# Performance work log

Measured on AMD Instinct MI355X. Metric: run time of the kernel, lower is better.

## Reference

```python
import jax, jax.numpy as jnp
import numpy as np

E, H, LQ, LC, B = 1024, 16, 1024, 512, 4
HD = E // H
FF = 4 * E
EPS = 1e-6


def _rope(x):
    # x: [B, H, L, D]; interleaved rotary embedding (lucidrains-style)
    D, L = x.shape[-1], x.shape[-2]
    inv_freq = 1.0 / (10000.0 ** (jnp.arange(0, D, 2, dtype=jnp.float32) / D))
    ang = jnp.arange(L, dtype=jnp.float32)[:, None] * inv_freq[None, :]  # [L, D/2]
    cos, sin = jnp.cos(ang), jnp.sin(ang)
    x1, x2 = x[..., 0::2], x[..., 1::2]
    r1 = x1 * cos - x2 * sin
    r2 = x1 * sin + x2 * cos
    return jnp.stack([r1, r2], axis=-1).reshape(x.shape)


def _ln(x, w, b):
    mu = jnp.mean(x, -1, keepdims=True)
    var = jnp.mean(jnp.square(x - mu), -1, keepdims=True)
    return (x - mu) * jax.lax.rsqrt(var + EPS) * w + b


def _rope_attn(x, ctx, qw, qb, kw, kb, vw, vb, pw, pb, mask):
    Bn, L, Em = x.shape
    Lc = ctx.shape[1]
    q = (x @ qw.T + qb).reshape(Bn, L, H, HD).transpose(0, 2, 1, 3)
    k = (ctx @ kw.T + kb).reshape(Bn, Lc, H, HD).transpose(0, 2, 1, 3)
    v = (ctx @ vw.T + vb).reshape(Bn, Lc, H, HD).transpose(0, 2, 1, 3)
    q, k = _rope(q), _rope(k)
    s = jnp.einsum('bhic,bhjc->bhij', q, k) / np.sqrt(HD).astype(np.float32)
    if mask is not None:
        s = jnp.where(mask[None, None], -jnp.inf, s)
    p = jax.nn.softmax(s, axis=-1)
    o = jnp.einsum('bhij,bhjc->bhic', p, v)
    o = o.transpose(0, 2, 1, 3).reshape(Bn, L, Em)
    return o @ pw.T + pb


def setup_inputs() -> dict:
    key = jax.random.key(0)
    ks = iter(jax.random.split(key, 40))
    s = 0.02
    d = {}
    d['x'] = jax.random.normal(next(ks), (B, LQ, E), jnp.float32)
    d['context'] = jax.random.normal(next(ks), (B, LC, E), jnp.float32)
    d['attn_mask'] = jnp.triu(jnp.ones((LQ, LQ), bool), k=1)  # True = masked (causal)
    for g in ('g_msa', 'g_ca', 'g_mlp'):
        d[g] = jax.random.normal(next(ks), (1, 1, E), jnp.float32) * s
    for n in ('n1', 'n2', 'n3'):
        d[n + '_w'] = jnp.ones((E,), jnp.float32)
        d[n + '_b'] = jnp.zeros((E,), jnp.float32)
    for p in ('sa', 'ca'):
        for m in ('q', 'k', 'v', 'p'):
            d[f'{p}_{m}w'] = jax.random.normal(next(ks), (E, E), jnp.float32) * s
            d[f'{p}_{m}b'] = jnp.zeros((E,), jnp.float32)
    d['fc1_w'] = jax.random.normal(next(ks), (FF, E), jnp.float32) * s
    d['fc1_b'] = jnp.zeros((FF,), jnp.float32)
    d['fc2_w'] = jax.random.normal(next(ks), (E, FF), jnp.float32) * s
    d['fc2_b'] = jnp.zeros((E,), jnp.float32)
    return d


def reference(x, context, attn_mask,
              g_msa, g_ca, g_mlp,
              n1_w, n1_b, n2_w, n2_b, n3_w, n3_b,
              sa_qw, sa_qb, sa_kw, sa_kb, sa_vw, sa_vb, sa_pw, sa_pb,
              ca_qw, ca_qb, ca_kw, ca_kb, ca_vw, ca_vb, ca_pw, ca_pb,
              fc1_w, fc1_b, fc2_w, fc2_b):
    # self-attention (causal RoPE) with zero-init learned gate
    x = x + g_msa * _rope_attn(_ln(x, n1_w, n1_b), _ln(x, n1_w, n1_b),
                               sa_qw, sa_qb, sa_kw, sa_kb, sa_vw, sa_vb,
                               sa_pw, sa_pb, attn_mask)
    # cross-attention (RoPE on both streams, no mask)
    h = _ln(x, n2_w, n2_b)
    x = x + g_ca * _rope_attn(h, context,
                              ca_qw, ca_qb, ca_kw, ca_kb, ca_vw, ca_vb,
                              ca_pw, ca_pb, None)
    # gated MLP with tanh-approx GELU
    h = _ln(x, n3_w, n3_b)
    h = jax.nn.gelu(h @ fc1_w.T + fc1_b, approximate=True) @ fc2_w.T + fc2_b
    x = x + g_mlp * h
    return x
```

## Files before the change

### kernel.cpp

```cpp
#include <hip/hip_runtime.h>
#include <math.h>

#if !__has_builtin(__builtin_amdgcn_cvt_pk_fp8_f32)
#include <hip/hip_fp8.h>
#endif

typedef __attribute__((ext_vector_type(8))) short short8;
typedef __attribute__((ext_vector_type(4))) float f32x4;
typedef __attribute__((ext_vector_type(16))) float f32x16;
typedef unsigned char u8;
typedef unsigned short u16;
typedef unsigned int u32;
typedef __attribute__((ext_vector_type(2))) u32 u32x2;
typedef __attribute__((ext_vector_type(4))) u32 u32x4;
typedef __attribute__((ext_vector_type(8))) int i32x8;
typedef unsigned long long u64;

static constexpr int E = 1024, H = 16, LQ = 1024, LC = 512, Bn = 4, FF = 4096;
static constexpr int NTOK = Bn * LQ;
static constexpr int NCTX = Bn * LC;

#define QSCALE 0.1803368801111244f
#define DEFER_THR 11.5f

static constexpr size_t OFF_TCOS   = 0;
static constexpr size_t OFF_TSIN   = OFF_TCOS + (size_t)LQ*32*4;
static constexpr size_t OFF_BSAQKV = OFF_TSIN + (size_t)LQ*32*4;
static constexpr size_t OFF_BCAKV  = OFF_BSAQKV + 16384;
static constexpr size_t OFF_WSAQKV = OFF_BCAKV + 16384;
static constexpr size_t OFF_WSAP   = OFF_WSAQKV + (size_t)3072*1024*2;
static constexpr size_t OFF_WCAQ   = OFF_WSAP   + (size_t)1024*1024*2;
static constexpr size_t OFF_WCAKV  = OFF_WCAQ   + (size_t)1024*1024*2;
static constexpr size_t OFF_WCAP   = OFF_WCAKV  + (size_t)2048*1024*2;
static constexpr size_t OFF_WFC1   = OFF_WCAP   + (size_t)1024*1024*2;
static constexpr size_t OFF_WFC2   = OFF_WFC1   + (size_t)4096*1024*2;
static constexpr size_t OFF_CTXB   = OFF_WFC2   + (size_t)1024*4096*2;
static constexpr size_t OFF_H      = OFF_CTXB   + (size_t)2048*1024*2;
static constexpr size_t OFF_QKV    = OFF_H      + (size_t)4096*1024*2;
static constexpr size_t OFF_CAQ    = OFF_QKV;
static constexpr size_t OFF_CAKV   = OFF_QKV + (size_t)4096*1024*2;
static constexpr size_t OFF_QR     = OFF_QKV + (size_t)4096*3072*2;
static constexpr size_t OFF_KR     = OFF_QR  + (size_t)4096*1024*2;
static constexpr size_t OFF_VT     = OFF_KR  + (size_t)4096*1024*2;
static constexpr size_t OFF_AO     = OFF_VT  + (size_t)4096*1024*2;
static constexpr size_t OFF_U      = OFF_QKV;
static constexpr size_t WS_NEED    = OFF_AO + (size_t)4096*1024*2;

static __device__ __forceinline__ float bf2f(u16 u) {
  union { u32 i; float f; } un; un.i = ((u32)u) << 16; return un.f;
}
static __device__ __forceinline__ u16 f2bf(float f) {
  union { float f; u32 u; } un; un.f = f;
  u32 u = un.u;
  return (u16)((u + 0x7FFFu + ((u >> 16) & 1u)) >> 16);
}
static __device__ __forceinline__ u64 pack4(u16 a, u16 b, u16 c, u16 d) {
  return (u64)a | ((u64)b << 16) | ((u64)c << 32) | ((u64)d << 48);
}
static __device__ __forceinline__ f32x4 mfma16(short8 a, short8 b, f32x4 c) {
  return __builtin_amdgcn_mfma_f32_16x16x32_bf16(a, b, c, 0, 0, 0);
}
static __device__ __forceinline__ f32x16 mfma32(short8 a, short8 b, f32x16 c) {
  return __builtin_amdgcn_mfma_f32_32x32x16_bf16(a, b, c, 0, 0, 0);
}
static __device__ __forceinline__ void gload_lds16(void* lds, const void* g) {
  __builtin_amdgcn_global_load_lds(
      (const __attribute__((address_space(1))) void*)g,
      (__attribute__((address_space(3))) void*)lds, 16, 0, 0);
}
static __device__ __forceinline__ float gelu_tanh(float x) {
  float z2 = 1.5957691216057308f * (x + 0.044715f * x * x * x);
  float e = __expf(z2);
  float r = __builtin_amdgcn_rcpf(e + 1.0f);
  return x - x * r;
}
static __device__ __forceinline__ u32 cvtpk_bf16(float lo, float hi) {
  u32 r;
  asm("v_cvt_pk_bf16_f32 %0, %1, %2" : "=v"(r) : "v"(lo), "v"(hi));
  return r;
}
static __device__ __forceinline__ u32 pack_fp8x4(float a, float b, float c, float d) {
#if __has_builtin(__builtin_amdgcn_cvt_pk_fp8_f32)
  u32 r = (u32)__builtin_amdgcn_cvt_pk_fp8_f32(a, b, 0, false);
  r = (u32)__builtin_amdgcn_cvt_pk_fp8_f32(c, d, (int)r, true);
  return r;
#else
  __hip_fp8_e4m3 qa(a), qb(b), qc(c), qd(d);
  return (u32)qa.__x | ((u32)qb.__x << 8) | ((u32)qc.__x << 16) | ((u32)qd.__x << 24);
#endif
}
static __device__ __forceinline__ u8 fp8b(float f) {
#if __has_builtin(__builtin_amdgcn_cvt_pk_fp8_f32)
  return (u8)((u32)__builtin_amdgcn_cvt_pk_fp8_f32(f, f, 0, false) & 0xFFu);
#else
  __hip_fp8_e4m3 t(f); return t.__x;
#endif
}

__global__ __launch_bounds__(256) void build_tab(float* __restrict__ ct, float* __restrict__ st) {
  int idx = blockIdx.x * 256 + threadIdx.x;
  int pos = idx >> 5, i = idx & 31;
  float inv = powf(10000.f, -(float)i * (1.f / 32.f));
  float a = (float)pos * inv;
  ct[idx] = cosf(a);
  st[idx] = sinf(a);
}

struct Cvt11 { const float* s[11]; };
__global__ __launch_bounds__(256) void cvt_all(Cvt11 a, u16* __restrict__ dst) {
  u32 gid = blockIdx.x * 256 + threadIdx.x;
  u32 s, off;
  if (gid < 2097152u)      { s = gid >> 18;                        off = gid & 262143u; }
  else if (gid < 4194304u) { return; }
  else                     { s = 10;                               off = gid - 4194304u; }
  float4 v = *(const float4*)(a.s[s] + (size_t)off * 4);
  *(u64*)(dst + (size_t)gid * 4) = pack4(f2bf(v.x), f2bf(v.y), f2bf(v.z), f2bf(v.w));
}

__global__ __launch_bounds__(256) void cvt_fp8(const float* __restrict__ s0, const float* __restrict__ s1,
                                               u8* __restrict__ d0, u8* __restrict__ d1) {
  u32 gid = blockIdx.x * 256 + threadIdx.x;
  const float* s; u8* d; u32 off;
  if (gid < 1048576u) { s = s0; d = d0; off = gid; }
  else                { s = s1; d = d1; off = gid - 1048576u; }
  float4 v = *(const float4*)(s + (size_t)off * 4);
  *(u32*)(d + (size_t)off * 4) =
      pack_fp8x4(v.x * 256.f, v.y * 256.f, v.z * 256.f, v.w * 256.f);
}

struct Cp5 { const float* s[5]; };
__global__ __launch_bounds__(256) void copy5(Cp5 a, float* __restrict__ dst) {
  int gid = blockIdx.x * 256 + threadIdx.x;
  int s = gid >> 10, off = gid & 1023;
  int doff = (s < 3) ? s * 1024 : 4096 + (s - 3) * 1024;
  dst[doff + off] = a.s[s][off];
}

__global__ __launch_bounds__(256) void init_bias_gate(float* __restrict__ out, const float* __restrict__ bias,
                                                      const float* __restrict__ gate) {
  int i = (blockIdx.x * 256 + threadIdx.x) * 4;
  int c = i & 1023;
  float4 o = *(float4*)(out + i);
  o.x += gate[c] * bias[c];
  o.y += gate[c + 1] * bias[c + 1];
  o.z += gate[c + 2] * bias[c + 2];
  o.w += gate[c + 3] * bias[c + 3];
  *(float4*)(out + i) = o;
}

__global__ __launch_bounds__(256) void ln_bf16(const float* __restrict__ x, const float* __restrict__ w,
                                               const float* __restrict__ b, u16* __restrict__ out) {
  __shared__ float red[4];
  int row = blockIdx.x, tid = threadIdx.x;
  const float* xr = x + (size_t)row * 1024;
  float4 v = ((const float4*)xr)[tid];
  float s = v.x + v.y + v.z + v.w;
#pragma unroll
  for (int off = 32; off; off >>= 1) s += __shfl_xor(s, off);
  if ((tid & 63) == 0) red[tid >> 6] = s;
  __syncthreads();
  float mean = (red[0] + red[1] + red[2] + red[3]) * (1.f / 1024.f);
  float dx = v.x - mean, dy = v.y - mean, dz = v.z - mean, dw = v.w - mean;
  float sq = dx * dx + dy * dy + dz * dz + dw * dw;
#pragma unroll
  for (int off = 32; off; off >>= 1) sq += __shfl_xor(sq, off);
  __syncthreads();
  if ((tid & 63) == 0) red[tid >> 6] = sq;
  __syncthreads();
  float var = (red[0] + red[1] + red[2] + red[3]) * (1.f / 1024.f);
  float rstd = rsqrtf(var + 1e-6f);
  float4 wv = ((const float4*)w)[tid];
  float4 bv = ((const float4*)b)[tid];
  u64 o = pack4(f2bf(dx * rstd * wv.x + bv.x), f2bf(dy * rstd * wv.y + bv.y),
                f2bf(dz * rstd * wv.z + bv.z), f2bf(dw * rstd * wv.w + bv.w));
  *(u64*)(out + (size_t)row * 1024 + tid * 4) = o;
}

__global__ __launch_bounds__(256) void ln_fp8(const float* __restrict__ x, const float* __restrict__ w,
                                              const float* __restrict__ b, u8* __restrict__ out) {
  __shared__ float red[4];
  int row = blockIdx.x, tid = threadIdx.x;
  const float* xr = x + (size_t)row * 1024;
  float4 v = ((const float4*)xr)[tid];
  float s = v.x + v.y + v.z + v.w;
#pragma unroll
  for (int off = 32; off; off >>= 1) s += __shfl_xor(s, off);
  if ((tid & 63) == 0) red[tid >> 6] = s;
  __syncthreads();
  float mean = (red[0] + red[1] + red[2] + red[3]) * (1.f / 1024.f);
  float dx = v.x - mean, dy = v.y - mean, dz = v.z - mean, dw = v.w - mean;
  float sq = dx * dx + dy * dy + dz * dz + dw * dw;
#pragma unroll
  for (int off = 32; off; off >>= 1) sq += __shfl_xor(sq, off);
  __syncthreads();
  if ((tid & 63) == 0) red[tid >> 6] = sq;
  __syncthreads();
  float var = (red[0] + red[1] + red[2] + red[3]) * (1.f / 1024.f);
  float rstd = rsqrtf(var + 1e-6f);
  float4 wv = ((const float4*)w)[tid];
  float4 bv = ((const float4*)b)[tid];
  u32 pk = pack_fp8x4((dx * rstd * wv.x + bv.x) * 16.f, (dy * rstd * wv.y + bv.y) * 16.f,
                      (dz * rstd * wv.z + bv.z) * 16.f, (dw * rstd * wv.w + bv.w) * 16.f);
  *(u32*)(out + (size_t)row * 1024 + tid * 4) = pk;
}

struct RopeJob { const u16* src; u16* dst; int ld, col0, Lper, T, mode; float scale; };
struct Rope3 { RopeJob j[3]; };
__global__ __launch_bounds__(128) void rope3(Rope3 a, const float* __restrict__ cosT,
                                             const float* __restrict__ sinT) {
  RopeJob jb = a.j[blockIdx.y];
  int t = blockIdx.x;
  if (t >= jb.T) return;
  int b = t / jb.Lper, l = t - b * jb.Lper;
  int tid = threadIdx.x;
  int e0 = tid * 8;
  int h = e0 >> 6, d0 = e0 & 63;
  short8 vv = *(const short8*)(jb.src + (size_t)t * jb.ld + jb.col0 + e0);
  if (jb.mode == 0) {
    short8 ov;
#pragma unroll
    for (int j = 0; j < 4; ++j) {
      float x1 = bf2f((u16)vv[2 * j]);
      float x2 = bf2f((u16)vv[2 * j + 1]);
      int i = (d0 >> 1) + j;
      float c = cosT[l * 32 + i], s = sinT[l * 32 + i];
      ov[2 * j]     = (short)f2bf((x1 * c - x2 * s) * jb.scale);
      ov[2 * j + 1] = (short)f2bf((x1 * s + x2 * c) * jb.scale);
    }
    *(short8*)(jb.dst + (((size_t)b * H + h) * jb.Lper + l) * 64 + d0) = ov;
  } else {
#pragma unroll
    for (int m = 0; m < 8; ++m)
      jb.dst[(((size_t)b * H + h) * 64 + d0 + m) * jb.Lper + l] = (u16)vv[m];
  }
}

enum { EPI_BF16 = 0, EPI_GELU = 1, EPI_RESID = 2, EPI_ATOMIC = 3 };

template <int EPI>
__global__ __launch_bounds__(512, 4) void gemm2(const u16* __restrict__ A, const u16* __restrict__ W,
                                                const float* __restrict__ bias, u16* outb, float* outf,
                                                const float* res, const float* __restrict__ gate,
                                                int M, int N, int K, int kchunks) {
  __shared__ u16 As[2][128 * 64];
  __shared__ u16 Bs[2][128 * 64];

  int nwg = gridDim.x * gridDim.y;
  int bid = blockIdx.y * gridDim.x + blockIdx.x;
  int cpx = nwg >> 3;
  int swz = (bid & 7) * cpx + (bid >> 3);
  int bx = swz % gridDim.x;
  int by = swz / gridDim.x;
  int row0 = by * 128, col0 = bx * 128;

  const int Kc = K / kchunks;
  const int kbase = blockIdx.z * Kc;

  int tid = threadIdx.x;
  int lane = tid & 63, wid = tid >> 6;
  int wr = wid >> 2, wc = wid & 3;
  int lr = lane & 15, lg = lane >> 4;

  size_t a_off0, a_off1, b_off0, b_off1;
  int l_off0 = tid * 8, l_off1 = (512 + tid) * 8;
  {
    int q = tid, r = q >> 3, p = q & 7, sp = p ^ (r & 7);
    a_off0 = (size_t)(row0 + r) * K + sp * 8;
    b_off0 = (size_t)(col0 + r) * K + sp * 8;
    q = 512 + tid; r = q >> 3; p = q & 7; sp = p ^ (r & 7);
    a_off1 = (size_t)(row0 + r) * K + sp * 8;
    b_off1 = (size_t)(col0 + r) * K + sp * 8;
  }

  f32x4 acc[4][2] = {};

  const int nkt = Kc >> 6;
  {
    gload_lds16(&As[0][l_off0], A + a_off0 + kbase);
    gload_lds16(&Bs[0][l_off0], W + b_off0 + kbase);
    gload_lds16(&As[0][l_off1], A + a_off1 + kbase);
    gload_lds16(&Bs[0][l_off1], W + b_off1 + kbase);
  }
  __syncthreads();

  for (int kt = 0; kt < nkt; ++kt) {
    int cur = kt & 1;
    if (kt + 1 < nkt) {
      int k0 = kbase + ((kt + 1) << 6);
      gload_lds16(&As[cur ^ 1][l_off0], A + a_off0 + k0);
      gload_lds16(&Bs[cur ^ 1][l_off0], W + b_off0 + k0);
      gload_lds16(&As[cur ^ 1][l_off1], A + a_off1 + k0);
      gload_lds16(&Bs[cur ^ 1][l_off1], W + b_off1 + k0);
    }
#pragma unroll
    for (int kk = 0; kk < 2; ++kk) {
      short8 af[4], bfr[2];
#pragma unroll
      for (int m = 0; m < 4; ++m) {
        int r = wr * 64 + m * 16 + lr;
        int sc = (kk * 4 + lg) ^ (r & 7);
        af[m] = *(const short8*)(&As[cur][r * 64 + sc * 8]);
      }
#pragma unroll
      for (int n = 0; n < 2; ++n) {
        int r = wc * 32 + n * 16 + lr;
        int sc = (kk * 4 + lg) ^ (r & 7);
        bfr[n] = *(const short8*)(&Bs[cur][r * 64 + sc * 8]);
      }
#pragma unroll
      for (int m = 0; m < 4; ++m)
#pragma unroll
        for (int n = 0; n < 2; ++n)
          acc[m][n] = mfma16(af[m], bfr[n], acc[m][n]);
    }
    __syncthreads();
  }

  if (EPI == EPI_BF16 || EPI == EPI_GELU) {
    u16* Ct = &As[0][0];
#pragma unroll
    for (int n = 0; n < 2; ++n) {
      int c = wc * 32 + n * 16 + lr;
      float bv = bias[col0 + c];
#pragma unroll
      for (int m = 0; m < 4; ++m) {
#pragma unroll
        for (int i = 0; i < 4; ++i) {
          int r = wr * 64 + m * 16 + lg * 4 + i;
          float v = acc[m][n][i] + bv;
          Ct[r * 128 + c] = f2bf(EPI == EPI_GELU ? gelu_tanh(v) : v);
        }
      }
    }
    __syncthreads();
#pragma unroll
    for (int j = 0; j < 4; ++j) {
      u32 q = (u32)tid + j * 512;
      u32 r = q >> 4, ck = q & 15;
      short8 v = *(const short8*)(Ct + r * 128 + ck * 8);
      *(short8*)(outb + (size_t)(row0 + r) * N + col0 + ck * 8) = v;
    }
  } else {
#pragma unroll
    for (int n = 0; n < 2; ++n) {
      int cg = col0 + wc * 32 + n * 16 + lr;
      float bv = (EPI == EPI_ATOMIC) ? 0.f : bias[cg];
#pragma unroll
      for (int m = 0; m < 4; ++m) {
#pragma unroll
        for (int i = 0; i < 4; ++i) {
          int rg = row0 + wr * 64 + m * 16 + lg * 4 + i;
          float v = acc[m][n][i] + bv;
          if (EPI == EPI_RESID) {
            float r = res[(size_t)rg * N + cg];
            outf[(size_t)rg * N + cg] = r + gate[cg] * v;
          } else {
            atomicAdd(&outf[(size_t)rg * N + cg], gate[cg] * v);
          }
        }
      }
    }
  }
}

enum { E8_GELU = 0, E8_ATOMIC = 1 };

template <int EPI>
__global__ __launch_bounds__(256, 2) void gemm8(const u8* __restrict__ A, const u8* __restrict__ W,
                                                const float* __restrict__ bias, u8* outb, float* outf,
                                                const float* __restrict__ gate,
                                                int M, int N, int K, int kchunks) {
  __shared__ u8 As[2][128 * 128];
  __shared__ u8 Bs[2][128 * 128];

  int nwg = gridDim.x * gridDim.y;
  int bid = blockIdx.y * gridDim.x + blockIdx.x;
  int cpx = nwg >> 3;
  int swz = (bid & 7) * cpx + (bid >> 3);
  int bx = swz % gridDim.x, by = swz / gridDim.x;
  int row0 = by * 128, col0 = bx * 128;

  const int Kc = K / kchunks;
  const int kbase = blockIdx.z * Kc;

  int tid = threadIdx.x;
  int lane = tid & 63, wid = tid >> 6;
  int wr = wid >> 1, wc = wid & 1;
  int l31 = lane & 31, hi = lane >> 5;

  u32 aoff[4], boff[4];
  int ldso[4];
#pragma unroll
  for (int j = 0; j < 4; ++j) {
    int q = tid + j * 256;
    int r = q >> 3, p = q & 7, sp = p ^ (r & 7);
    aoff[j] = (u32)(row0 + r) * (u32)K + sp * 16;
    boff[j] = (u32)(col0 + r) * (u32)K + sp * 16;
    ldso[j] = q * 16;
  }

  f32x16 acc[2][2] = {};
  const int nkt = Kc >> 7;

  auto rdfrag = [&](const u8* base, int wbase, int ks, i32x8* f) {
#pragma unroll
    for (int blk = 0; blk < 2; ++blk) {
      int r = wbase + blk * 32 + l31;
      const u8* rp = base + r * 128;
      int ck = ks * 4 + hi * 2;
      u32x4 lo = *(const u32x4*)(rp + ((ck) ^ (r & 7)) * 16);
      u32x4 hh = *(const u32x4*)(rp + ((ck + 1) ^ (r & 7)) * 16);
      i32x8 v;
      v[0] = (int)lo[0]; v[1] = (int)lo[1]; v[2] = (int)lo[2]; v[3] = (int)lo[3];
      v[4] = (int)hh[0]; v[5] = (int)hh[1]; v[6] = (int)hh[2]; v[7] = (int)hh[3];
      f[blk] = v;
    }
  };

#pragma unroll
  for (int j = 0; j < 4; ++j) {
    gload_lds16(&As[0][ldso[j]], A + aoff[j] + kbase);
    gload_lds16(&Bs[0][ldso[j]], W + boff[j] + kbase);
  }
  __syncthreads();

  for (int kt = 0; kt < nkt; ++kt) {
    int cur = kt & 1;
    if (kt + 1 < nkt) {
      int k0 = kbase + ((kt + 1) << 7);
#pragma unroll
      for (int j = 0; j < 4; ++j) {
        gload_lds16(&As[cur ^ 1][ldso[j]], A + aoff[j] + k0);
        gload_lds16(&Bs[cur ^ 1][ldso[j]], W + boff[j] + k0);
      }
    }
#pragma unroll
    for (int ks = 0; ks < 2; ++ks) {
      i32x8 a[2], b[2];
      rdfrag(&As[cur][0], wr * 64, ks, a);
      rdfrag(&Bs[cur][0], wc * 64, ks, b);
      __builtin_amdgcn_s_setprio(1);
#pragma unroll
      for (int mi = 0; mi < 2; ++mi)
#pragma unroll
        for (int ni = 0; ni < 2; ++ni)
          acc[mi][ni] = __builtin_amdgcn_mfma_scale_f32_32x32x64_f8f6f4(
              a[mi], b[ni], acc[mi][ni], 0, 0, 0, 0x7F7F7F7F, 0, 0x7F7F7F7F);
      __builtin_amdgcn_s_setprio(0);
    }
    __syncthreads();
  }

  constexpr float SCL = 1.f / 4096.f;
  if (EPI == E8_GELU) {
    u8* Ct = &As[0][0];
#pragma unroll
    for (int ni = 0; ni < 2; ++ni) {
      int cl = wc * 64 + ni * 32 + l31;
      float bv = bias[col0 + cl];
#pragma unroll
      for (int mi = 0; mi < 2; ++mi) {
#pragma unroll
        for (int g = 0; g < 16; ++g) {
          int rl = wr * 64 + mi * 32 + (g & 3) + 8 * (g >> 2) + 4 * hi;
          float v = acc[mi][ni][g] * SCL + bv;
          Ct[rl * 128 + cl] = fp8b(gelu_tanh(v) * 16.f);
        }
      }
    }
    __syncthreads();
#pragma unroll
    for (int j = 0; j < 4; ++j) {
      int q = tid + j * 256;
      int r = q >> 3, ck = q & 7;
      *(u32x4*)(outb + (size_t)(row0 + r) * N + col0 + ck * 16) =
          *(const u32x4*)(Ct + r * 128 + ck * 16);
    }
  } else {
#pragma unroll
    for (int ni = 0; ni < 2; ++ni) {
      int cg = col0 + wc * 64 + ni * 32 + l31;
      float gv = gate[cg];
#pragma unroll
      for (int mi = 0; mi < 2; ++mi) {
#pragma unroll
        for (int g = 0; g < 16; ++g) {
          int rg = row0 + wr * 64 + mi * 32 + (g & 3) + 8 * (g >> 2) + 4 * hi;
          atomicAdd(&outf[(size_t)rg * N + cg], gv * (acc[mi][ni][g] * SCL));
        }
      }
    }
  }
}

template <int MASKED, int PRE>
static __device__ __forceinline__ void attn_tile3(short8* kf, const u16* KtNext,
                                                  const u16* Vp0, const u16* Vp1,
                                                  const short8* qf, int kb, int q0, int l31, int hi,
                                                  float& m, float& lsum, f32x16& o0, f32x16& o1) {
  short8 vf0[4], vf1[4];
#pragma unroll
  for (int ks = 0; ks < 4; ++ks) {
    vf0[ks] = *(const short8*)(Vp0 + ks * 16 + hi * 8);
    vf1[ks] = *(const short8*)(Vp1 + ks * 16 + hi * 8);
  }
  f32x16 s0 = {}, s1 = {};
  __builtin_amdgcn_s_setprio(1);
#pragma unroll
  for (int s = 0; s < 4; ++s) {
    s0 = mfma32(kf[s], qf[s], s0);
    s1 = mfma32(kf[4 + s], qf[s], s1);
  }
  __builtin_amdgcn_s_setprio(0);
  if (PRE) {
    const u16* kp0 = KtNext + (size_t)l31 * 64 + hi * 8;
    const u16* kp1 = KtNext + (size_t)(32 + l31) * 64 + hi * 8;
#pragma unroll
    for (int s = 0; s < 4; ++s) {
      kf[s] = *(const short8*)(kp0 + s * 16);
      kf[4 + s] = *(const short8*)(kp1 + s * 16);
    }
  }
  if (MASKED) {
    int qg = q0 + l31;
#pragma unroll
    for (int r = 0; r < 16; ++r) {
      int kk = kb + (r & 3) + 8 * (r >> 2) + 4 * hi;
      if (kk > qg) s0[r] = -INFINITY;
      if (kk + 32 > qg) s1[r] = -INFINITY;
    }
  }
  float pm = -INFINITY;
#pragma unroll
  for (int r = 0; r < 16; ++r) pm = fmaxf(pm, fmaxf(s0[r], s1[r]));
  pm = fmaxf(pm, __shfl_xor(pm, 32));
  if (!__all(pm <= m + DEFER_THR)) {
    float mn = fmaxf(m, pm);
    float al = exp2f(m - mn);
    m = mn;
    lsum *= al;
#pragma unroll
    for (int r = 0; r < 16; ++r) {
      float alr = __shfl(al, (r & 3) + 8 * (r >> 2) + 4 * hi);
      o0[r] *= alr;
      o1[r] *= alr;
    }
  }
  float ts = 0.f;
#pragma unroll
  for (int r = 0; r < 16; ++r) {
    float p0 = exp2f(s0[r] - m);
    float p1 = exp2f(s1[r] - m);
    s0[r] = p0; s1[r] = p1;
    ts += p0 + p1;
  }
  ts += __shfl_xor(ts, 32);
  lsum += ts;
  auto pack8 = [&](float a0, float a1, float a2, float a3,
                   float a4, float a5, float a6, float a7) -> short8 {
    u32 c0 = cvtpk_bf16(a0, a1), c1 = cvtpk_bf16(a2, a3);
    u32 c2 = cvtpk_bf16(a4, a5), c3 = cvtpk_bf16(a6, a7);
    u32x2 r02 = __builtin_amdgcn_permlane32_swap(c0, c2, false, false);
    u32x2 r13 = __builtin_amdgcn_permlane32_swap(c1, c3, false, false);
    u32x4 w;
    w[0] = r02[0]; w[1] = r13[0]; w[2] = r02[1]; w[3] = r13[1];
    return __builtin_bit_cast(short8, w);
  };
  short8 pa0 = pack8(s0[0], s0[1], s0[2], s0[3], s0[4], s0[5], s0[6], s0[7]);
  short8 pa1 = pack8(s0[8], s0[9], s0[10], s0[11], s0[12], s0[13], s0[14], s0[15]);
  short8 pa2 = pack8(s1[0], s1[1], s1[2], s1[3], s1[4], s1[5], s1[6], s1[7]);
  short8 pa3 = pack8(s1[8], s1[9], s1[10], s1[11], s1[12], s1[13], s1[14], s1[15]);
  short8 pa[4] = {pa0, pa1, pa2, pa3};
  __builtin_amdgcn_s_setprio(1);
#pragma unroll
  for (int ks = 0; ks < 4; ++ks) {
    o0 = mfma32(pa[ks], vf0[ks], o0);
    o1 = mfma32(pa[ks], vf1[ks], o1);
  }
  __builtin_amdgcn_s_setprio(0);
}

template <int CAUSAL>
__global__ __launch_bounds__(256) void flash_attn2(const u16* __restrict__ Q, const u16* __restrict__ K,
                                                   const u16* __restrict__ Vt, u16* __restrict__ O,
                                                   int Lq, int Lk) {
  const int wid = threadIdx.x >> 6, lane = threadIdx.x & 63;
  const int l31 = lane & 31, hi = lane >> 5;
  int wg = blockIdx.x * 4 + wid;
  int bh = wg & 63;
  int qc = wg >> 6;
  if (CAUSAL) qc = (Lq >> 5) - 1 - qc;
  int q0 = qc << 5;

  const u16* Qb = Q + ((size_t)bh * Lq + q0) * 64;
  const u16* Kb = K + (size_t)bh * Lk * 64;
  const u16* Vb = Vt + (size_t)bh * 64 * Lk;

  short8 qf[4];
#pragma unroll
  for (int s = 0; s < 4; ++s) qf[s] = *(const short8*)(Qb + (size_t)l31 * 64 + s * 16 + hi * 8);

  f32x16 o0 = {}, o1 = {};
  float m = -INFINITY, lsum = 0.f;

  const u16* Kt = Kb;
  const u16* Vp0 = Vb + (size_t)l31 * Lk;
  const u16* Vp1 = Vb + (size_t)(32 + l31) * Lk;

  short8 kf[8];
  {
    const u16* kp0 = Kt + (size_t)l31 * 64 + hi * 8;
    const u16* kp1 = Kt + (size_t)(32 + l31) * 64 + hi * 8;
#pragma unroll
    for (int s = 0; s < 4; ++s) {
      kf[s] = *(const short8*)(kp0 + s * 16);
      kf[4 + s] = *(const short8*)(kp1 + s * 16);
    }
  }

  int nt = CAUSAL ? ((q0 >> 6) + 1) : (Lk >> 6);
  for (int t = 0; t < nt - 1; ++t) {
    attn_tile3<0, 1>(kf, Kt + 64 * 64, Vp0, Vp1, qf, t * 64, q0, l31, hi, m, lsum, o0, o1);
    Kt += 64 * 64; Vp0 += 64; Vp1 += 64;
  }
  if (CAUSAL)
    attn_tile3<1, 0>(kf, nullptr, Vp0, Vp1, qf, (nt - 1) * 64, q0, l31, hi, m, lsum, o0, o1);
  else
    attn_tile3<0, 0>(kf, nullptr, Vp0, Vp1, qf, (nt - 1) * 64, q0, l31, hi, m, lsum, o0, o1);

  float myinv = 1.f / lsum;
  int b = bh >> 4, h = bh & 15;
#pragma unroll
  for (int r = 0; r < 16; ++r) {
    int cr = (r & 3) + 8 * (r >> 2) + 4 * hi;
    float li = __shfl(myinv, cr);
    u16* op = O + ((size_t)b * Lq + q0 + cr) * 1024 + h * 64;
    op[l31] = f2bf(o0[r] * li);
    op[32 + l31] = f2bf(o1[r] * li);
  }
}

extern "C" void kernel_launch(void* const* d_in, const int* in_sizes, int n_in,
                              void* d_out, int out_size, void* d_ws, size_t ws_size,
                              hipStream_t stream) {
  (void)in_sizes; (void)n_in; (void)out_size;
  if (ws_size < WS_NEED) return;

  const float* x     = (const float*)d_in[0];
  const float* ctx   = (const float*)d_in[1];
  const float* g_msa = (const float*)d_in[3];
  const float* g_ca  = (const float*)d_in[4];
  const float* g_mlp = (const float*)d_in[5];
  const float* n1w = (const float*)d_in[6],  *n1b = (const float*)d_in[7];
  const float* n2w = (const float*)d_in[8],  *n2b = (const float*)d_in[9];
  const float* n3w = (const float*)d_in[10], *n3b = (const float*)d_in[11];
  const float* sa_qw = (const float*)d_in[12], *sa_kw = (const float*)d_in[14];
  const float* sa_vw = (const float*)d_in[16], *sa_pw = (const float*)d_in[18];
  const float* sa_qb = (const float*)d_in[13], *sa_kb = (const float*)d_in[15];
  const float* sa_vb = (const float*)d_in[17], *sa_pb = (const float*)d_in[19];
  const float* ca_qw = (const float*)d_in[20], *ca_qb = (const float*)d_in[21];
  const float* ca_kw = (const float*)d_in[22], *ca_kb = (const float*)d_in[23];
  const float* ca_vw = (const float*)d_in[24], *ca_vb = (const float*)d_in[25];
  const float* ca_pw = (const float*)d_in[26], *ca_pb = (const float*)d_in[27];
  const float* fc1w = (const float*)d_in[28], *fc1b = (const float*)d_in[29];
  const float* fc2w = (const float*)d_in[30], *fc2b = (const float*)d_in[31];

  char* ws = (char*)d_ws;
  float* out = (float*)d_out;
  float* tcos = (float*)(ws + OFF_TCOS);
  float* tsin = (float*)(ws + OFF_TSIN);
  u16* Hb   = (u16*)(ws + OFF_H);
  u16* QKV  = (u16*)(ws + OFF_QKV);
  u16* QR   = (u16*)(ws + OFF_QR);
  u16* KR   = (u16*)(ws + OFF_KR);
  u16* VT   = (u16*)(ws + OFF_VT);
  u16* AO   = (u16*)(ws + OFF_AO);
  u8*  H8   = (u8*)(ws + OFF_H);
  u8*  U8   = (u8*)(ws + OFF_U);
  u8*  W8FC1 = (u8*)(ws + OFF_QR);
  u8*  W8FC2 = (u8*)(ws + OFF_KR);

  build_tab<<<dim3(128), dim3(256), 0, stream>>>(tcos, tsin);

  Cvt11 ca;
  ca.s[0] = sa_qw; ca.s[1] = sa_kw; ca.s[2] = sa_vw; ca.s[3] = sa_pw;
  ca.s[4] = ca_qw; ca.s[5] = ca_kw; ca.s[6] = ca_vw; ca.s[7] = ca_pw;
  ca.s[8] = fc1w;  ca.s[9] = fc2w;  ca.s[10] = ctx;
  cvt_all<<<dim3(18432), dim3(256), 0, stream>>>(ca, (u16*)(ws + OFF_WSAQKV));
  Cp5 cp;
  cp.s[0] = sa_qb; cp.s[1] = sa_kb; cp.s[2] = sa_vb; cp.s[3] = ca_kb; cp.s[4] = ca_vb;
  copy5<<<dim3(20), dim3(256), 0, stream>>>(cp, (float*)(ws + OFF_BSAQKV));

  ln_bf16<<<dim3(NTOK), dim3(256), 0, stream>>>(x, n1w, n1b, Hb);
  gemm2<EPI_BF16><<<dim3(3072 / 128, NTOK / 128), dim3(512), 0, stream>>>(
      Hb, (u16*)(ws + OFF_WSAQKV), (float*)(ws + OFF_BSAQKV), QKV, nullptr, nullptr, nullptr,
      NTOK, 3072, 1024, 1);
  {
    Rope3 r;
    r.j[0] = {QKV, QR, 3072, 0,    LQ, NTOK, 0, QSCALE};
    r.j[1] = {QKV, KR, 3072, 1024, LQ, NTOK, 0, 1.0f};
    r.j[2] = {QKV, VT, 3072, 2048, LQ, NTOK, 1, 1.0f};
    rope3<<<dim3(NTOK, 3), dim3(128), 0, stream>>>(r, tcos, tsin);
  }
  flash_attn2<1><<<dim3(512), dim3(256), 0, stream>>>(QR, KR, VT, AO, LQ, LQ);
  gemm2<EPI_RESID><<<dim3(1024 / 128, NTOK / 128), dim3(512), 0, stream>>>(
      AO, (u16*)(ws + OFF_WSAP), sa_pb, nullptr, out, x, g_msa, NTOK, 1024, 1024, 1);

  ln_bf16<<<dim3(NTOK), dim3(256), 0, stream>>>(out, n2w, n2b, Hb);
  gemm2<EPI_BF16><<<dim3(1024 / 128, NTOK / 128), dim3(512), 0, stream>>>(
      Hb, (u16*)(ws + OFF_WCAQ), ca_qb, (u16*)(ws + OFF_CAQ), nullptr, nullptr, nullptr,
      NTOK, 1024, 1024, 1);
  gemm2<EPI_BF16><<<dim3(2048 / 128, NCTX / 128), dim3(512), 0, stream>>>(
      (u16*)(ws + OFF_CTXB), (u16*)(ws + OFF_WCAKV), (float*)(ws + OFF_BCAKV),
      (u16*)(ws + OFF_CAKV), nullptr, nullptr, nullptr, NCTX, 2048, 1024, 1);
  {
    Rope3 r;
    r.j[0] = {(u16*)(ws + OFF_CAQ),  QR, 1024, 0,    LQ, NTOK, 0, QSCALE};
    r.j[1] = {(u16*)(ws + OFF_CAKV), KR, 2048, 0,    LC, NCTX, 0, 1.0f};
    r.j[2] = {(u16*)(ws + OFF_CAKV), VT, 2048, 1024, LC, NCTX, 1, 1.0f};
    rope3<<<dim3(NTOK, 3), dim3(128), 0, stream>>>(r, tcos, tsin);
  }
  flash_attn2<0><<<dim3(512), dim3(256), 0, stream>>>(QR, KR, VT, AO, LQ, LC);
  gemm2<EPI_RESID><<<dim3(1024 / 128, NTOK / 128), dim3(512), 0, stream>>>(
      AO, (u16*)(ws + OFF_WCAP), ca_pb, nullptr, out, out, g_ca, NTOK, 1024, 1024, 1);

  cvt_fp8<<<dim3(8192), dim3(256), 0, stream>>>(fc1w, fc2w, W8FC1, W8FC2);
  ln_fp8<<<dim3(NTOK), dim3(256), 0, stream>>>(out, n3w, n3b, H8);
  gemm8<E8_GELU><<<dim3(4096 / 128, NTOK / 128), dim3(256), 0, stream>>>(
      H8, W8FC1, fc1b, U8, nullptr, nullptr, NTOK, 4096, 1024, 1);
  init_bias_gate<<<dim3(4096), dim3(256), 0, stream>>>(out, fc2b, g_mlp);
  gemm8<E8_ATOMIC><<<dim3(1024 / 128, NTOK / 128, 2), dim3(256), 0, stream>>>(
      U8, W8FC2, nullptr, nullptr, out, g_mlp, NTOK, 1024, 4096, 2);
}
```

Baseline: 389.5 us.

## Replace split-K atomic FC2 with fused residual epilogue and 16x16x128 FP8 MFMA

The FC2 GEMM no longer uses a two-way split-K with atomicAdd plus a separate bias/gate init kernel. It now runs a single pass that writes residual + gate*(acc+bias) directly. The FP8 GEMM's inner loop also switches from 32x32x64 scaled MFMA to 16x16x128, with a 4x4 accumulator grid per wave, changing how fragments are read from LDS. Dropping split-K removes atomics and one kernel launch, but halves the FC2 grid to 256 blocks, which may underfill the GPU over the long K=4096 loop.

```diff
diff --git a/kernel.cpp b/kernel.cpp
--- a/kernel.cpp
+++ b/kernel.cpp
@@ -136,18 +136,6 @@
   dst[doff + off] = a.s[s][off];
 }
 
-__global__ __launch_bounds__(256) void init_bias_gate(float* __restrict__ out, const float* __restrict__ bias,
-                                                      const float* __restrict__ gate) {
-  int i = (blockIdx.x * 256 + threadIdx.x) * 4;
-  int c = i & 1023;
-  float4 o = *(float4*)(out + i);
-  o.x += gate[c] * bias[c];
-  o.y += gate[c + 1] * bias[c + 1];
-  o.z += gate[c + 2] * bias[c + 2];
-  o.w += gate[c + 3] * bias[c + 3];
-  *(float4*)(out + i) = o;
-}
-
 __global__ __launch_bounds__(256) void ln_bf16(const float* __restrict__ x, const float* __restrict__ w,
                                                const float* __restrict__ b, u16* __restrict__ out) {
   __shared__ float red[4];
@@ -235,13 +223,13 @@
   }
 }
 
-enum { EPI_BF16 = 0, EPI_GELU = 1, EPI_RESID = 2, EPI_ATOMIC = 3 };
+enum { EPI_BF16 = 0, EPI_GELU = 1, EPI_RESID = 2 };
 
 template <int EPI>
 __global__ __launch_bounds__(512, 4) void gemm2(const u16* __restrict__ A, const u16* __restrict__ W,
                                                 const float* __restrict__ bias, u16* outb, float* outf,
                                                 const float* res, const float* __restrict__ gate,
-                                                int M, int N, int K, int kchunks) {
+                                                int M, int N, int K) {
   __shared__ u16 As[2][128 * 64];
   __shared__ u16 Bs[2][128 * 64];
 
@@ -252,9 +240,6 @@
   int bx = swz % gridDim.x;
   int by = swz / gridDim.x;
   int row0 = by * 128, col0 = bx * 128;
-
-  const int Kc = K / kchunks;
-  const int kbase = blockIdx.z * Kc;
 
   int tid = threadIdx.x;
   int lane = tid & 63, wid = tid >> 6;
@@ -274,19 +259,19 @@
 
   f32x4 acc[4][2] = {};
 
-  const int nkt = Kc >> 6;
+  const int nkt = K >> 6;
   {
-    gload_lds16(&As[0][l_off0], A + a_off0 + kbase);
-    gload_lds16(&Bs[0][l_off0], W + b_off0 + kbase);
-    gload_lds16(&As[0][l_off1], A + a_off1 + kbase);
-    gload_lds16(&Bs[0][l_off1], W + b_off1 + kbase);
+    gload_lds16(&As[0][l_off0], A + a_off0);
+    gload_lds16(&Bs[0][l_off0], W + b_off0);
+    gload_lds16(&As[0][l_off1], A + a_off1);
+    gload_lds16(&Bs[0][l_off1], W + b_off1);
   }
   __syncthreads();
 
   for (int kt = 0; kt < nkt; ++kt) {
     int cur = kt & 1;
     if (kt + 1 < nkt) {
-      int k0 = kbase + ((kt + 1) << 6);
+      int k0 = (kt + 1) << 6;
       gload_lds16(&As[cur ^ 1][l_off0], A + a_off0 + k0);
       gload_lds16(&Bs[cur ^ 1][l_off0], W + b_off0 + k0);
       gload_lds16(&As[cur ^ 1][l_off1], A + a_off1 + k0);
@@ -344,32 +329,28 @@
 #pragma unroll
     for (int n = 0; n < 2; ++n) {
       int cg = col0 + wc * 32 + n * 16 + lr;
-      float bv = (EPI == EPI_ATOMIC) ? 0.f : bias[cg];
+      float bv = bias[cg];
 #pragma unroll
       for (int m = 0; m < 4; ++m) {
 #pragma unroll
         for (int i = 0; i < 4; ++i) {
           int rg = row0 + wr * 64 + m * 16 + lg * 4 + i;
           float v = acc[m][n][i] + bv;
-          if (EPI == EPI_RESID) {
-            float r = res[(size_t)rg * N + cg];
-            outf[(size_t)rg * N + cg] = r + gate[cg] * v;
-          } else {
-            atomicAdd(&outf[(size_t)rg * N + cg], gate[cg] * v);
-          }
+          float r = res[(size_t)rg * N + cg];
+          outf[(size_t)rg * N + cg] = r + gate[cg] * v;
         }
       }
     }
   }
 }
 
-enum { E8_GELU = 0, E8_ATOMIC = 1 };
+enum { E8_GELU = 0, E8_RESID = 1 };
 
 template <int EPI>
 __global__ __launch_bounds__(256, 2) void gemm8(const u8* __restrict__ A, const u8* __restrict__ W,
                                                 const float* __restrict__ bias, u8* outb, float* outf,
-                                                const float* __restrict__ gate,
-                                                int M, int N, int K, int kchunks) {
+                                                const float* res, const float* __restrict__ gate,
+                                                int M, int N, int K) {
   __shared__ u8 As[2][128 * 128];
   __shared__ u8 Bs[2][128 * 128];
 
@@ -380,13 +361,10 @@
   int bx = swz % gridDim.x, by = swz / gridDim.x;
   int row0 = by * 128, col0 = bx * 128;
 
-  const int Kc = K / kchunks;
-  const int kbase = blockIdx.z * Kc;
-
   int tid = threadIdx.x;
   int lane = tid & 63, wid = tid >> 6;
   int wr = wid >> 1, wc = wid & 1;
-  int l31 = lane & 31, hi = lane >> 5;
+  int lr = lane & 15, lg = lane >> 4;
 
   u32 aoff[4], boff[4];
   int ldso[4];
@@ -399,55 +377,50 @@
     ldso[j] = q * 16;
   }
 
-  f32x16 acc[2][2] = {};
-  const int nkt = Kc >> 7;
-
-  auto rdfrag = [&](const u8* base, int wbase, int ks, i32x8* f) {
-#pragma unroll
-    for (int blk = 0; blk < 2; ++blk) {
-      int r = wbase + blk * 32 + l31;
-      const u8* rp = base + r * 128;
-      int ck = ks * 4 + hi * 2;
-      u32x4 lo = *(const u32x4*)(rp + ((ck) ^ (r & 7)) * 16);
-      u32x4 hh = *(const u32x4*)(rp + ((ck + 1) ^ (r & 7)) * 16);
-      i32x8 v;
-      v[0] = (int)lo[0]; v[1] = (int)lo[1]; v[2] = (int)lo[2]; v[3] = (int)lo[3];
-      v[4] = (int)hh[0]; v[5] = (int)hh[1]; v[6] = (int)hh[2]; v[7] = (int)hh[3];
-      f[blk] = v;
-    }
+  f32x4 acc[4][4] = {};
+  const int nkt = K >> 7;
+
+  auto rdfrag = [&](const u8* base, int r, i32x8& f) {
+    const u8* rp = base + r * 128;
+    int ck = lg * 2;
+    u32x4 lo = *(const u32x4*)(rp + ((ck) ^ (r & 7)) * 16);
+    u32x4 hh = *(const u32x4*)(rp + ((ck + 1) ^ (r & 7)) * 16);
+    i32x8 v;
+    v[0] = (int)lo[0]; v[1] = (int)lo[1]; v[2] = (int)lo[2]; v[3] = (int)lo[3];
+    v[4] = (int)hh[0]; v[5] = (int)hh[1]; v[6] = (int)hh[2]; v[7] = (int)hh[3];
+    f = v;
   };
 
 #pragma unroll
   for (int j = 0; j < 4; ++j) {
-    gload_lds16(&As[0][ldso[j]], A + aoff[j] + kbase);
-    gload_lds16(&Bs[0][ldso[j]], W + boff[j] + kbase);
+    gload_lds16(&As[0][ldso[j]], A + aoff[j]);
+    gload_lds16(&Bs[0][ldso[j]], W + boff[j]);
   }
   __syncthreads();
 
   for (int kt = 0; kt < nkt; ++kt) {
     int cur = kt & 1;
     if (kt + 1 < nkt) {
-      int k0 = kbase + ((kt + 1) << 7);
+      int k0 = (kt + 1) << 7;
 #pragma unroll
       for (int j = 0; j < 4; ++j) {
         gload_lds16(&As[cur ^ 1][ldso[j]], A + aoff[j] + k0);
         gload_lds16(&Bs[cur ^ 1][ldso[j]], W + boff[j] + k0);
       }
     }
-#pragma unroll
-    for (int ks = 0; ks < 2; ++ks) {
-      i32x8 a[2], b[2];
-      rdfrag(&As[cur][0], wr * 64, ks, a);
-      rdfrag(&Bs[cur][0], wc * 64, ks, b);
-      __builtin_amdgcn_s_setprio(1);
-#pragma unroll
-      for (int mi = 0; mi < 2; ++mi)
-#pragma unroll
-        for (int ni = 0; ni < 2; ++ni)
-          acc[mi][ni] = __builtin_amdgcn_mfma_scale_f32_32x32x64_f8f6f4(
-              a[mi], b[ni], acc[mi][ni], 0, 0, 0, 0x7F7F7F7F, 0, 0x7F7F7F7F);
-      __builtin_amdgcn_s_setprio(0);
-    }
+    i32x8 a[4], b[4];
+#pragma unroll
+    for (int m = 0; m < 4; ++m) rdfrag(&As[cur][0], wr * 64 + m * 16 + lr, a[m]);
+#pragma unroll
+    for (int n = 0; n < 4; ++n) rdfrag(&Bs[cur][0], wc * 64 + n * 16 + lr, b[n]);
+    __builtin_amdgcn_s_setprio(1);
+#pragma unroll
+    for (int m = 0; m < 4; ++m)
+#pragma unroll
+      for (int n = 0; n < 4; ++n)
+        acc[m][n] = __builtin_amdgcn_mfma_scale_f32_16x16x128_f8f6f4(
+            a[m], b[n], acc[m][n], 0, 0, 0, 0x7F7F7F7F, 0, 0x7F7F7F7F);
+    __builtin_amdgcn_s_setprio(0);
     __syncthreads();
   }
 
@@ -455,15 +428,15 @@
   if (EPI == E8_GELU) {
     u8* Ct = &As[0][0];
 #pragma unroll
-    for (int ni = 0; ni < 2; ++ni) {
-      int cl = wc * 64 + ni * 32 + l31;
+    for (int n = 0; n < 4; ++n) {
+      int cl = wc * 64 + n * 16 + lr;
       float bv = bias[col0 + cl];
 #pragma unroll
-      for (int mi = 0; mi < 2; ++mi) {
-#pragma unroll
-        for (int g = 0; g < 16; ++g) {
-          int rl = wr * 64 + mi * 32 + (g & 3) + 8 * (g >> 2) + 4 * hi;
-          float v = acc[mi][ni][g] * SCL + bv;
+      for (int m = 0; m < 4; ++m) {
+#pragma unroll
+        for (int i = 0; i < 4; ++i) {
+          int rl = wr * 64 + m * 16 + lg * 4 + i;
+          float v = acc[m][n][i] * SCL + bv;
           Ct[rl * 128 + cl] = fp8b(gelu_tanh(v) * 16.f);
         }
       }
@@ -478,15 +451,17 @@
     }
   } else {
 #pragma unroll
-    for (int ni = 0; ni < 2; ++ni) {
-      int cg = col0 + wc * 64 + ni * 32 + l31;
-      float gv = gate[cg];
-#pragma unroll
-      for (int mi = 0; mi < 2; ++mi) {
-#pragma unroll
-        for (int g = 0; g < 16; ++g) {
-          int rg = row0 + wr * 64 + mi * 32 + (g & 3) + 8 * (g >> 2) + 4 * hi;
-          atomicAdd(&outf[(size_t)rg * N + cg], gv * (acc[mi][ni][g] * SCL));
+    for (int n = 0; n < 4; ++n) {
+      int cg = col0 + wc * 64 + n * 16 + lr;
+      float bv = bias[cg], gv = gate[cg];
+#pragma unroll
+      for (int m = 0; m < 4; ++m) {
+#pragma unroll
+        for (int i = 0; i < 4; ++i) {
+          int rg = row0 + wr * 64 + m * 16 + lg * 4 + i;
+          float v = acc[m][n][i] * SCL + bv;
+          float r = res[(size_t)rg * N + cg];
+          outf[(size_t)rg * N + cg] = r + gv * v;
         }
       }
     }
@@ -694,7 +669,7 @@
   ln_bf16<<<dim3(NTOK), dim3(256), 0, stream>>>(x, n1w, n1b, Hb);
   gemm2<EPI_BF16><<<dim3(3072 / 128, NTOK / 128), dim3(512), 0, stream>>>(
       Hb, (u16*)(ws + OFF_WSAQKV), (float*)(ws + OFF_BSAQKV), QKV, nullptr, nullptr, nullptr,
-      NTOK, 3072, 1024, 1);
+      NTOK, 3072, 1024);
   {
     Rope3 r;
     r.j[0] = {QKV, QR, 3072, 0,    LQ, NTOK, 0, QSCALE};
@@ -704,15 +679,15 @@
   }
   flash_attn2<1><<<dim3(512), dim3(256), 0, stream>>>(QR, KR, VT, AO, LQ, LQ);
   gemm2<EPI_RESID><<<dim3(1024 / 128, NTOK / 128), dim3(512), 0, stream>>>(
-      AO, (u16*)(ws + OFF_WSAP), sa_pb, nullptr, out, x, g_msa, NTOK, 1024, 1024, 1);
+      AO, (u16*)(ws + OFF_WSAP), sa_pb, nullptr, out, x, g_msa, NTOK, 1024, 1024);
 
   ln_bf16<<<dim3(NTOK), dim3(256), 0, stream>>>(out, n2w, n2b, Hb);
   gemm2<EPI_BF16><<<dim3(1024 / 128, NTOK / 128), dim3(512), 0, stream>>>(
       Hb, (u16*)(ws + OFF_WCAQ), ca_qb, (u16*)(ws + OFF_CAQ), nullptr, nullptr, nullptr,
-      NTOK, 1024, 1024, 1);
+      NTOK, 1024, 1024);
   gemm2<EPI_BF16><<<dim3(2048 / 128, NCTX / 128), dim3(512), 0, stream>>>(
       (u16*)(ws + OFF_CTXB), (u16*)(ws + OFF_WCAKV), (float*)(ws + OFF_BCAKV),
-      (u16*)(ws + OFF_CAKV), nullptr, nullptr, nullptr, NCTX, 2048, 1024, 1);
+      (u16*)(ws + OFF_CAKV), nullptr, nullptr, nullptr, NCTX, 2048, 1024);
   {
     Rope3 r;
     r.j[0] = {(u16*)(ws + OFF_CAQ),  QR, 1024, 0,    LQ, NTOK, 0, QSCALE};
@@ -722,13 +697,12 @@
   }
   flash_attn2<0><<<dim3(512), dim3(256), 0, stream>>>(QR, KR, VT, AO, LQ, LC);
   gemm2<EPI_RESID><<<dim3(1024 / 128, NTOK / 128), dim3(512), 0, stream>>>(
-      AO, (u16*)(ws + OFF_WCAP), ca_pb, nullptr, out, out, g_ca, NTOK, 1024, 1024, 1);
+      AO, (u16*)(ws + OFF_WCAP), ca_pb, nullptr, out, out, g_ca, NTOK, 1024, 1024);
 
   cvt_fp8<<<dim3(8192), dim3(256), 0, stream>>>(fc1w, fc2w, W8FC1, W8FC2);
   ln_fp8<<<dim3(NTOK), dim3(256), 0, stream>>>(out, n3w, n3b, H8);
   gemm8<E8_GELU><<<dim3(4096 / 128, NTOK / 128), dim3(256), 0, stream>>>(
-      H8, W8FC1, fc1b, U8, nullptr, nullptr, NTOK, 4096, 1024, 1);
-  init_bias_gate<<<dim3(4096), dim3(256), 0, stream>>>(out, fc2b, g_mlp);
-  gemm8<E8_ATOMIC><<<dim3(1024 / 128, NTOK / 128, 2), dim3(256), 0, stream>>>(
-      U8, W8FC2, nullptr, nullptr, out, g_mlp, NTOK, 1024, 4096, 2);
-}
+      H8, W8FC1, fc1b, U8, nullptr, nullptr, nullptr, NTOK, 4096, 1024);
+  gemm8<E8_RESID><<<dim3(1024 / 128, NTOK / 128), dim3(256), 0, stream>>>(
+      U8, W8FC2, fc2b, nullptr, out, out, g_mlp, NTOK, 1024, 4096);
+}
```

New measurement: 380.1 us. -2.4%, faster.
